# Kernel optimization log

Hardware: AMD Instinct MI355X
Metric: run time of the kernel (lower is better)

Reference implementation:

```python
import jax, jax.numpy as jnp
import numpy as np

B, M = 512, 2048            # batch of src-tgt pairs, sampled walk positions per pair
NUM_KEYS = 1_000_000        # unique (node, time) keys in nodetime2emb map
NUM_NODES = 100_000
LP = 4                      # num_layers + 1 (saw encoding width)
ENC = 32                    # enc_dim
FEAT = 64                   # node feature dim (MergeLayer dim2)
D3, D4 = 64, 1              # MergeLayer hidden / output dims


def setup_inputs() -> dict:
    key = jax.random.key(0)
    ks = jax.random.split(key, 12)
    s = 0.05
    return {
        "pos_table": jax.random.uniform(ks[0], (NUM_KEYS, LP), dtype=jnp.float32),
        "node_feat": jax.random.normal(ks[1], (NUM_NODES, FEAT), dtype=jnp.float32),
        "W1": jax.random.normal(ks[2], (LP, ENC), dtype=jnp.float32) * s,
        "b1": jnp.zeros((ENC,), dtype=jnp.float32),
        "W2": jax.random.normal(ks[3], (ENC, ENC), dtype=jnp.float32) * s,
        "b2": jnp.zeros((ENC,), dtype=jnp.float32),
        "Wm1": jax.random.normal(ks[4], (ENC + FEAT, D3), dtype=jnp.float32) * s,
        "bm1": jnp.zeros((D3,), dtype=jnp.float32),
        "Wm2": jax.random.normal(ks[5], (D3, D4), dtype=jnp.float32) * s,
        "bm2": jnp.zeros((D4,), dtype=jnp.float32),
        "key_idx": jax.random.randint(ks[6], (B, M), 0, NUM_KEYS, dtype=jnp.int32),
        "node_idx": jax.random.randint(ks[7], (B, M), 0, NUM_NODES, dtype=jnp.int32),
    }


def reference(pos_table, node_feat, W1, b1, W2, b2, Wm1, bm1, Wm2, bm2, key_idx, node_idx):
    # PositionEncoder.forward: gather saw encodings by (node, time) key,
    # then trainable_embedding = Linear(LP->ENC) -> ReLU -> Linear(ENC->ENC)
    enc = pos_table[key_idx]                       # [B, M, LP] irregular gather
    pe = jax.nn.relu(enc @ W1 + b1) @ W2 + b2      # [B, M, ENC]
    # gather raw node features for the same walk positions
    feat = node_feat[node_idx]                     # [B, M, FEAT] irregular gather
    # MergeLayer (non_linear=True): concat -> fc1 -> ReLU -> fc2
    x = jnp.concatenate([pe, feat], axis=-1)       # [B, M, ENC+FEAT]
    z = jax.nn.relu(x @ Wm1 + bm1) @ Wm2 + bm2     # [B, M, 1]
    return z
```

## Files before the change

kernel.cpp:

```cpp
#include <hip/hip_runtime.h>


typedef _Float16 half8 __attribute__((ext_vector_type(8)));
typedef float floatx4 __attribute__((ext_vector_type(4)));

#define HSTR 40
#define WSTR 104
#define GRID_MAIN 768

__global__ void feat_to_f16(const float* __restrict__ nf,
                            _Float16* __restrict__ o, int n8) {
    int t = blockIdx.x * 256 + threadIdx.x;
    if (t >= n8) return;
    const float4* p = (const float4*)nf + (size_t)t * 2;
    const float4 a = p[0], b = p[1];
    half8 h;
    h[0] = (_Float16)a.x; h[1] = (_Float16)a.y;
    h[2] = (_Float16)a.z; h[3] = (_Float16)a.w;
    h[4] = (_Float16)b.x; h[5] = (_Float16)b.y;
    h[6] = (_Float16)b.z; h[7] = (_Float16)b.w;
    *((half8*)o + t) = h;
}

__global__ __launch_bounds__(256, 3) void neurtw_r10(
    const float* __restrict__ pos_table,
    const float* __restrict__ node_feat,
    const float* __restrict__ W1,
    const float* __restrict__ b1,
    const float* __restrict__ W2,
    const float* __restrict__ b2,
    const float* __restrict__ Wm1,
    const float* __restrict__ bm1,
    const float* __restrict__ Wm2,
    const float* __restrict__ bm2,
    const int*   __restrict__ key_idx,
    const int*   __restrict__ node_idx,
    const _Float16* __restrict__ feat16,
    int use_f16,
    float*       __restrict__ out,
    int rows)
{
    __shared__ _Float16 hpe[256 * HSTR];
    __shared__ _Float16 wm1t[64 * WSTR];

    const int tid  = threadIdx.x;
    const int lane = tid & 63;
    const int r0   = (tid >> 6) * 64;
    const int ln   = lane & 15;
    const int q    = lane >> 4;

    #pragma unroll
    for (int i = 0; i < 3; ++i) {
        const int task = i * 256 + tid;
        const int n = task & 63, k8 = task >> 6;
        half8 w;
        #pragma unroll
        for (int kk = 0; kk < 8; ++kk)
            w[kk] = (_Float16)Wm1[(k8 * 8 + kk) * 64 + n];
        *(half8*)(&wm1t[n * WSTR + k8 * 8]) = w;
    }

    half8 b_w2[2];
    #pragma unroll
    for (int ct = 0; ct < 2; ++ct)
        #pragma unroll
        for (int j = 0; j < 8; ++j)
            b_w2[ct][j] = (_Float16)W2[(q * 8 + j) * 32 + ct * 16 + ln];
    float b2v[2];
    b2v[0] = b2[ln]; b2v[1] = b2[16 + ln];
    float bm1v[4], wm2v[4];
    #pragma unroll
    for (int ct = 0; ct < 4; ++ct) {
        bm1v[ct] = bm1[ct * 16 + ln];
        wm2v[ct] = Wm2[ct * 16 + ln];
    }
    const float bm2s = bm2[0];

    __syncthreads();

    for (int base = blockIdx.x * 256; base < rows; base += GRID_MAIN * 256) {
        const int row = base + tid;

        int ndr[4];
        #pragma unroll
        for (int rt = 0; rt < 4; ++rt)
            ndr[rt] = node_idx[base + r0 + rt * 16 + ln];

        half8 fA[4][2];
        if (use_f16) {
            #pragma unroll
            for (int rt = 0; rt < 4; ++rt) {
                const _Float16* fb = feat16 + (size_t)ndr[rt] * 64 + q * 8;
                fA[rt][0] = *(const half8*)(fb);
                fA[rt][1] = *(const half8*)(fb + 32);
            }
        } else {
            #pragma unroll
            for (int rt = 0; rt < 4; ++rt) {
                const float* fb = node_feat + (size_t)ndr[rt] * 64 + q * 8;
                #pragma unroll
                for (int kt = 0; kt < 2; ++kt) {
                    const float4 lo = *(const float4*)(fb + kt * 32);
                    const float4 hi = *(const float4*)(fb + kt * 32 + 4);
                    half8 h;
                    h[0] = (_Float16)lo.x; h[1] = (_Float16)lo.y;
                    h[2] = (_Float16)lo.z; h[3] = (_Float16)lo.w;
                    h[4] = (_Float16)hi.x; h[5] = (_Float16)hi.y;
                    h[6] = (_Float16)hi.z; h[7] = (_Float16)hi.w;
                    fA[rt][kt] = h;
                }
            }
        }

        const int kk = key_idx[row];
        const float4 enc = *(const float4*)(pos_table + (size_t)kk * 4);

        #pragma unroll
        for (int g = 0; g < 4; ++g) {
            half8 hv;
            #pragma unroll
            for (int j8 = 0; j8 < 8; ++j8) {
                const int j = g * 8 + j8;
                float a = fmaf(enc.w, W1[96 + j],
                          fmaf(enc.z, W1[64 + j],
                          fmaf(enc.y, W1[32 + j],
                          fmaf(enc.x, W1[j], b1[j]))));
                hv[j8] = (_Float16)fmaxf(a, 0.0f);
            }
            *(half8*)(&hpe[tid * HSTR + g * 8]) = hv;
        }
        half8 a_h[4];
        #pragma unroll
        for (int rt = 0; rt < 4; ++rt)
            a_h[rt] = *(const half8*)(&hpe[(r0 + rt * 16 + ln) * HSTR + q * 8]);

        floatx4 pc[4][2];
        #pragma unroll
        for (int rt = 0; rt < 4; ++rt)
            #pragma unroll
            for (int ct = 0; ct < 2; ++ct) {
                floatx4 c = {0.f, 0.f, 0.f, 0.f};
                pc[rt][ct] = __builtin_amdgcn_mfma_f32_16x16x32_f16(
                    a_h[rt], b_w2[ct], c, 0, 0, 0);
            }

        #pragma unroll
        for (int rt = 0; rt < 4; ++rt)
            #pragma unroll
            for (int ct = 0; ct < 2; ++ct)
                #pragma unroll
                for (int r = 0; r < 4; ++r)
                    hpe[(r0 + rt * 16 + q * 4 + r) * HSTR + ct * 16 + ln] =
                        (_Float16)(pc[rt][ct][r] + b2v[ct]);

        floatx4 acc[4][4];
        #pragma unroll
        for (int ct = 0; ct < 4; ++ct) {
            const float bb = bm1v[ct];
            #pragma unroll
            for (int rt = 0; rt < 4; ++rt)
                acc[rt][ct] = (floatx4){bb, bb, bb, bb};
        }

        {
            half8 a_pe[4];
            #pragma unroll
            for (int rt = 0; rt < 4; ++rt)
                a_pe[rt] = *(const half8*)(&hpe[(r0 + rt * 16 + ln) * HSTR + q * 8]);
            half8 b0[4];
            #pragma unroll
            for (int ct = 0; ct < 4; ++ct)
                b0[ct] = *(const half8*)(&wm1t[(ct * 16 + ln) * WSTR + q * 8]);
            #pragma unroll
            for (int rt = 0; rt < 4; ++rt)
                #pragma unroll
                for (int ct = 0; ct < 4; ++ct)
                    acc[rt][ct] = __builtin_amdgcn_mfma_f32_16x16x32_f16(
                        a_pe[rt], b0[ct], acc[rt][ct], 0, 0, 0);
        }

        #pragma unroll
        for (int kt = 0; kt < 2; ++kt) {
            half8 bk[4];
            #pragma unroll
            for (int ct = 0; ct < 4; ++ct)
                bk[ct] = *(const half8*)(&wm1t[(ct * 16 + ln) * WSTR + 32 + kt * 32 + q * 8]);
            #pragma unroll
            for (int rt = 0; rt < 4; ++rt)
                #pragma unroll
                for (int ct = 0; ct < 4; ++ct)
                    acc[rt][ct] = __builtin_amdgcn_mfma_f32_16x16x32_f16(
                        fA[rt][kt], bk[ct], acc[rt][ct], 0, 0, 0);
        }

        #pragma unroll
        for (int rt = 0; rt < 4; ++rt) {
            #pragma unroll
            for (int r = 0; r < 4; ++r) {
                float p = 0.0f;
                #pragma unroll
                for (int ct = 0; ct < 4; ++ct)
                    p = fmaf(fmaxf(acc[rt][ct][r], 0.0f), wm2v[ct], p);
                p += __shfl_xor(p, 1);
                p += __shfl_xor(p, 2);
                p += __shfl_xor(p, 4);
                p += __shfl_xor(p, 8);
                if (ln == 0)
                    out[base + r0 + rt * 16 + q * 4 + r] = p + bm2s;
            }
        }
    }
}

extern "C" void kernel_launch(void* const* d_in, const int* in_sizes, int n_in,
                              void* d_out, int out_size, void* d_ws, size_t ws_size,
                              hipStream_t stream) {
    const float* pos_table = (const float*)d_in[0];
    const float* node_feat = (const float*)d_in[1];
    const float* W1        = (const float*)d_in[2];
    const float* b1        = (const float*)d_in[3];
    const float* W2        = (const float*)d_in[4];
    const float* b2        = (const float*)d_in[5];
    const float* Wm1       = (const float*)d_in[6];
    const float* bm1       = (const float*)d_in[7];
    const float* Wm2       = (const float*)d_in[8];
    const float* bm2       = (const float*)d_in[9];
    const int*   key_idx   = (const int*)d_in[10];
    const int*   node_idx  = (const int*)d_in[11];
    float* out = (float*)d_out;

    const int rows  = in_sizes[10];
    const int nfeat = in_sizes[1];

    _Float16* feat16 = (_Float16*)d_ws;
    const size_t need = (size_t)nfeat * sizeof(_Float16);
    const int use_f16 = (ws_size >= need) ? 1 : 0;

    if (use_f16) {
        const int n8 = nfeat / 8;
        feat_to_f16<<<(n8 + 255) / 256, 256, 0, stream>>>(node_feat, feat16, n8);
    }

    neurtw_r10<<<GRID_MAIN, 256, 0, stream>>>(
        pos_table, node_feat, W1, b1, W2, b2, Wm1, bm1, Wm2, bm2,
        key_idx, node_idx, feat16, use_f16, out, rows);
}
```

Measured before the change: 157.4 us.

## Bucket rows by node index before gather to improve feature-table locality

Adds a per-call counting sort (histogram, scan, scatter) that groups rows by coarse node-index bucket, so the main kernel's node-feature gathers hit nearby rows of the fp16 feature table and reuse L2 more. The main kernel reads permuted node/key arrays and scatters results back through a row permutation. This costs three extra launches, extra passes over the index arrays, atomics, and scattered output writes, and the key-table gather stays random.

```diff
diff --git a/kernel.cpp b/kernel.cpp
--- a/kernel.cpp
+++ b/kernel.cpp
@@ -9,20 +9,84 @@
 #define GRID_MAIN 768
 
 __global__ void feat_to_f16(const float* __restrict__ nf,
-                            _Float16* __restrict__ o, int n8) {
-    int t = blockIdx.x * 256 + threadIdx.x;
-    if (t >= n8) return;
-    const float4* p = (const float4*)nf + (size_t)t * 2;
-    const float4 a = p[0], b = p[1];
-    half8 h;
-    h[0] = (_Float16)a.x; h[1] = (_Float16)a.y;
-    h[2] = (_Float16)a.z; h[3] = (_Float16)a.w;
-    h[4] = (_Float16)b.x; h[5] = (_Float16)b.y;
-    h[6] = (_Float16)b.z; h[7] = (_Float16)b.w;
-    *((half8*)o + t) = h;
-}
-
-__global__ __launch_bounds__(256, 3) void neurtw_r10(
+                            _Float16* __restrict__ o, int n8,
+                            unsigned* __restrict__ hist, int bins) {
+    if (blockIdx.x == 0)
+        for (int b = threadIdx.x; b < bins; b += 256) hist[b] = 0u;
+    for (int t = blockIdx.x * 256 + threadIdx.x; t < n8; t += gridDim.x * 256) {
+        const float4* p = (const float4*)nf + (size_t)t * 2;
+        const float4 a = p[0], b = p[1];
+        half8 h;
+        h[0] = (_Float16)a.x; h[1] = (_Float16)a.y;
+        h[2] = (_Float16)a.z; h[3] = (_Float16)a.w;
+        h[4] = (_Float16)b.x; h[5] = (_Float16)b.y;
+        h[6] = (_Float16)b.z; h[7] = (_Float16)b.w;
+        *((half8*)o + t) = h;
+    }
+}
+
+__global__ __launch_bounds__(256) void g1_hist(
+    const int* __restrict__ node_idx, int rows,
+    unsigned* __restrict__ hist, int bins, int shift) {
+    __shared__ unsigned lh[1024];
+    for (int b = threadIdx.x; b < bins; b += 256) lh[b] = 0u;
+    __syncthreads();
+    for (int r = blockIdx.x * 256 + threadIdx.x; r < rows; r += gridDim.x * 256)
+        atomicAdd(&lh[((unsigned)node_idx[r]) >> shift], 1u);
+    __syncthreads();
+    for (int b = threadIdx.x; b < bins; b += 256)
+        if (lh[b]) atomicAdd(&hist[b], lh[b]);
+}
+
+__global__ __launch_bounds__(1024) void g2_scan(
+    const unsigned* __restrict__ hist, unsigned* __restrict__ cursor, int bins) {
+    __shared__ unsigned s[1024];
+    const int t = threadIdx.x;
+    const unsigned own = (t < bins) ? hist[t] : 0u;
+    s[t] = own;
+    __syncthreads();
+    #pragma unroll
+    for (int off = 1; off < 1024; off <<= 1) {
+        unsigned v = (t >= off) ? s[t - off] : 0u;
+        __syncthreads();
+        s[t] += v;
+        __syncthreads();
+    }
+    if (t < bins) cursor[t] = s[t] - own;
+}
+
+__global__ __launch_bounds__(256) void g3_scatter(
+    const int* __restrict__ node_idx, const int* __restrict__ key_idx,
+    int rows, unsigned* __restrict__ cursor, int bins, int shift,
+    unsigned* __restrict__ pnode, unsigned* __restrict__ pkey,
+    unsigned* __restrict__ prow) {
+    __shared__ unsigned lh[1024];
+    __shared__ unsigned lbase[1024];
+    const int t = threadIdx.x;
+    const int R0 = blockIdx.x * 4096;
+    const int rend = (R0 + 4096 < rows) ? R0 + 4096 : rows;
+    for (int b = t; b < bins; b += 256) lh[b] = 0u;
+    __syncthreads();
+    for (int r = R0 + t; r < rend; r += 256)
+        atomicAdd(&lh[((unsigned)node_idx[r]) >> shift], 1u);
+    __syncthreads();
+    for (int b = t; b < bins; b += 256) {
+        const unsigned c = lh[b];
+        lbase[b] = c ? atomicAdd(&cursor[b], c) : 0u;
+    }
+    __syncthreads();
+    for (int r = R0 + t; r < rend; r += 256) {
+        const unsigned nd = (unsigned)node_idx[r];
+        const unsigned b  = nd >> shift;
+        const unsigned k  = atomicSub(&lh[b], 1u) - 1u;
+        const unsigned p  = lbase[b] + k;
+        pnode[p] = nd;
+        pkey[p]  = (unsigned)key_idx[r];
+        prow[p]  = (unsigned)r;
+    }
+}
+
+__global__ __launch_bounds__(256, 3) void neurtw_r13(
     const float* __restrict__ pos_table,
     const float* __restrict__ node_feat,
     const float* __restrict__ W1,
@@ -33,10 +97,11 @@
     const float* __restrict__ bm1,
     const float* __restrict__ Wm2,
     const float* __restrict__ bm2,
-    const int*   __restrict__ key_idx,
-    const int*   __restrict__ node_idx,
+    const unsigned* __restrict__ pnode,
+    const unsigned* __restrict__ pkey,
+    const unsigned* __restrict__ prow,
     const _Float16* __restrict__ feat16,
-    int use_f16,
+    int use_f16, int use_perm,
     float*       __restrict__ out,
     int rows)
 {
@@ -55,8 +120,8 @@
         const int n = task & 63, k8 = task >> 6;
         half8 w;
         #pragma unroll
-        for (int kk = 0; kk < 8; ++kk)
-            w[kk] = (_Float16)Wm1[(k8 * 8 + kk) * 64 + n];
+        for (int kk2 = 0; kk2 < 8; ++kk2)
+            w[kk2] = (_Float16)Wm1[(k8 * 8 + kk2) * 64 + n];
         *(half8*)(&wm1t[n * WSTR + k8 * 8]) = w;
     }
 
@@ -79,12 +144,10 @@
     __syncthreads();
 
     for (int base = blockIdx.x * 256; base < rows; base += GRID_MAIN * 256) {
-        const int row = base + tid;
-
         int ndr[4];
         #pragma unroll
         for (int rt = 0; rt < 4; ++rt)
-            ndr[rt] = node_idx[base + r0 + rt * 16 + ln];
+            ndr[rt] = (int)pnode[base + r0 + rt * 16 + ln];
 
         half8 fA[4][2];
         if (use_f16) {
@@ -112,7 +175,7 @@
             }
         }
 
-        const int kk = key_idx[row];
+        const int kk = (int)pkey[base + tid];
         const float4 enc = *(const float4*)(pos_table + (size_t)kk * 4);
 
         #pragma unroll
@@ -205,8 +268,11 @@
                 p += __shfl_xor(p, 2);
                 p += __shfl_xor(p, 4);
                 p += __shfl_xor(p, 8);
-                if (ln == 0)
-                    out[base + r0 + rt * 16 + q * 4 + r] = p + bm2s;
+                if (ln == 0) {
+                    const int pos = base + r0 + rt * 16 + q * 4 + r;
+                    const int orow = use_perm ? (int)prow[pos] : pos;
+                    out[orow] = p + bm2s;
+                }
             }
         }
     }
@@ -229,19 +295,45 @@
     const int*   node_idx  = (const int*)d_in[11];
     float* out = (float*)d_out;
 
-    const int rows  = in_sizes[10];
-    const int nfeat = in_sizes[1];
-
-    _Float16* feat16 = (_Float16*)d_ws;
-    const size_t need = (size_t)nfeat * sizeof(_Float16);
-    const int use_f16 = (ws_size >= need) ? 1 : 0;
+    const int rows   = in_sizes[10];
+    const int nfeat  = in_sizes[1];
+    const int nnodes = nfeat / 64;
+
+    int shift = 7;
+    while (((nnodes + (1 << shift) - 1) >> shift) > 1024) ++shift;
+    const int bins = (nnodes + (1 << shift) - 1) >> shift;
+
+    size_t off = 0;
+    _Float16* feat16 = (_Float16*)((char*)d_ws + off);
+    off += ((size_t)nfeat * 2 + 255) & ~(size_t)255;
+    unsigned* pnode = (unsigned*)((char*)d_ws + off); off += (size_t)rows * 4;
+    unsigned* pkey  = (unsigned*)((char*)d_ws + off); off += (size_t)rows * 4;
+    unsigned* prow  = (unsigned*)((char*)d_ws + off); off += (size_t)rows * 4;
+    unsigned* hist  = (unsigned*)((char*)d_ws + off); off += (size_t)bins * 4;
+    unsigned* cursor= (unsigned*)((char*)d_ws + off); off += (size_t)bins * 4;
+
+    const size_t need_f16  = (size_t)nfeat * 2;
+    const size_t need_full = off;
+    const int use_f16  = (ws_size >= need_f16) ? 1 : 0;
+    const int use_perm = (ws_size >= need_full && use_f16) ? 1 : 0;
 
     if (use_f16) {
         const int n8 = nfeat / 8;
-        feat_to_f16<<<(n8 + 255) / 256, 256, 0, stream>>>(node_feat, feat16, n8);
-    }
-
-    neurtw_r10<<<GRID_MAIN, 256, 0, stream>>>(
+        feat_to_f16<<<768, 256, 0, stream>>>(node_feat, feat16, n8,
+                                             hist, use_perm ? bins : 0);
+    }
+    if (use_perm) {
+        g1_hist<<<256, 256, 0, stream>>>(node_idx, rows, hist, bins, shift);
+        g2_scan<<<1, 1024, 0, stream>>>(hist, cursor, bins);
+        g3_scatter<<<(rows + 4095) / 4096, 256, 0, stream>>>(
+            node_idx, key_idx, rows, cursor, bins, shift, pnode, pkey, prow);
+    }
+
+    const unsigned* pn = use_perm ? pnode : (const unsigned*)node_idx;
+    const unsigned* pk = use_perm ? pkey  : (const unsigned*)key_idx;
+    const unsigned* pr = use_perm ? prow  : (const unsigned*)node_idx;
+
+    neurtw_r13<<<GRID_MAIN, 256, 0, stream>>>(
         pos_table, node_feat, W1, b1, W2, b2, Wm1, bm1, Wm2, bm2,
-        key_idx, node_idx, feat16, use_f16, out, rows);
-}
+        pn, pk, pr, feat16, use_f16, use_perm, out, rows);
+}
```

After: 239.4 us. +52.1%, slower.
